# Kernel tuning notes

Measured on AMD Instinct MI355X. Metric: run time of the kernel, lower is better.

The kernel has to match this reference:

```python
import jax, jax.numpy as jnp
import numpy as np

DIM = 384
HEADS = 12
K = 3          # kernel_size
PAD = 1
STRIDE = 1
B, H, W = 8, 56, 56


def conv1x1(x, w, b=None):
    # x: [B,C,H,W], w: [O,C]
    y = jnp.einsum('bchw,oc->bohw', x, w)
    if b is not None:
        y = y + b[None, :, None, None]
    return y


def unfold(x, k, p, s):
    # torch nn.Unfold: returns patches [B, C, k*k, nH, nW], kernel row-major, channel-major overall
    Bx, C, Hx, Wx = x.shape
    nH = (Hx + 2 * p - k) // s + 1
    nW = (Wx + 2 * p - k) // s + 1
    xp = jnp.pad(x, ((0, 0), (0, 0), (p, p), (p, p)))
    cols = [xp[:, :, i:i + s * nH:s, j:j + s * nW:s] for i in range(k) for j in range(k)]
    return jnp.stack(cols, axis=2), nH, nW


def fold(col, Hx, Wx, k, p, s):
    # torch F.fold (col2im): scatter-add overlapping windows. col: [B, C, k*k, nH, nW]
    Bx, C, _, nH, nW = col.shape
    canvas = jnp.zeros((Bx, C, Hx + 2 * p, Wx + 2 * p), col.dtype)
    idx = 0
    for i in range(k):
        for j in range(k):
            canvas = canvas.at[:, :, i:i + s * nH:s, j:j + s * nW:s].add(col[:, :, idx])
            idx += 1
    return canvas[:, :, p:p + Hx, p:p + Wx]


def setup_inputs() -> dict:
    key = jax.random.key(0)
    ks = jax.random.split(key, 5)
    k2 = K * K
    x = jax.random.normal(ks[0], (B, DIM, H, W), dtype=jnp.float32)
    v_w = jax.random.normal(ks[1], (DIM, DIM), dtype=jnp.float32) * 0.02
    v_b = jnp.zeros((DIM,), dtype=jnp.float32)
    attn_w = jax.random.normal(ks[2], (k2 * k2 * HEADS, DIM), dtype=jnp.float32) * 0.02
    proj_w = jax.random.normal(ks[3], (DIM, DIM), dtype=jnp.float32) * 0.02
    return {'x': x, 'v_w': v_w, 'v_b': v_b, 'attn_w': attn_w, 'proj_w': proj_w}


def reference(x, v_w, v_b, attn_w, proj_w):
    Bx, C, Hx, Wx = x.shape
    k2 = K * K
    hd = C // HEADS  # head dim
    # value projection + unfold into overlapping k x k windows
    v = conv1x1(x, v_w, v_b)
    vcol, nH, nW = unfold(v, K, PAD, STRIDE)        # [B, C, k2, nH, nW]
    L = nH * nW
    v = vcol.reshape(Bx, HEADS, hd, k2, L)          # split C = (heads, hd), heads slow
    v = v.transpose(0, 1, 4, 3, 2)                  # [B, n, L, k2(d), hd]
    # adaptive avg pool to (nH, nW); with stride=1 this is identity (pool window 1)
    ph, pw = Hx // nH, Wx // nW
    xp = x.reshape(Bx, C, nH, ph, nW, pw).mean(axis=(3, 5))
    # per-pixel attention logits, channel layout = ((i*k2 + d)*HEADS + head)
    a = jnp.einsum('bchw,oc->bohw', xp, attn_w)     # [B, k2*k2*n, nH, nW]
    a = a.reshape(Bx, k2, k2, HEADS, L)             # [B, i, d, n, L]
    a = a.transpose(0, 3, 4, 1, 2)                  # [B, n, L, i, d]
    a = jax.nn.softmax(a, axis=-1)
    out = jnp.einsum('bnlid,bnldh->bnlih', a, v)    # [B, n, L, i, hd]
    out = out.transpose(0, 1, 4, 3, 2)              # [B, n, hd, i, L] -> channel (n*hd+h)
    out = out.reshape(Bx, C, k2, nH, nW)
    out = fold(out, Hx, Wx, K, PAD, STRIDE)         # scatter-add windows back
    return conv1x1(out, proj_w)
```

## Files before the change

### kernel.cpp

```cpp
#include <hip/hip_runtime.h>
#include <hip/hip_bf16.h>

#define DIM   384
#define HEADS 12
#define K2    9
#define HH    56
#define WW    56
#define HWP   3136
#define BB    8
#define AO    972
#define AOP   976
#define MCAT  1408
#define PP    3200
#define PPAD  3600
#define W60   60

#define WBLK     2688
#define HALOBLK  696

typedef __hip_bfloat16 bf16;
typedef short bf16x8 __attribute__((ext_vector_type(8)));
typedef short bf16x4v __attribute__((ext_vector_type(4)));
typedef float f32x4 __attribute__((ext_vector_type(4)));
typedef float f32x2 __attribute__((ext_vector_type(2)));

static __device__ __forceinline__ float b2f(bf16 v) { return __bfloat162float(v); }
static __device__ __forceinline__ float bs2f(short s) {
    return __uint_as_float(((unsigned int)(unsigned short)s) << 16);
}
static __device__ __forceinline__ short f2bs(float f) {
    __hip_bfloat16 h = __float2bfloat16(f);
    return *(short*)&h;
}
static __device__ __forceinline__ f32x2 unpk(unsigned int u) {
    f32x2 r;
    r[0] = __uint_as_float(u << 16);
    r[1] = __uint_as_float(u & 0xffff0000u);
    return r;
}

static __device__ __forceinline__ void gl_lds16(const bf16* g, bf16* l) {
    __builtin_amdgcn_global_load_lds(
        (const __attribute__((address_space(1))) unsigned int*)g,
        (__attribute__((address_space(3))) unsigned int*)l, 16, 0, 0);
}

__global__ __launch_bounds__(256) void prep_kernel(
        const float* __restrict__ x, const float* __restrict__ v_w,
        const float* __restrict__ attn_w, const float* __restrict__ proj_w,
        bf16* __restrict__ xT, bf16* __restrict__ wcat, bf16* __restrict__ wp,
        bf16* __restrict__ vP) {
    const int bid = blockIdx.x;
    if (bid < 400) {
        const int lane = threadIdx.x & 63, w = threadIdx.x >> 6;
        const int p = (bid % 50) * 64 + lane;
        const int b = bid / 50;
        bf16* dst = xT + ((size_t)b * PP + p) * DIM;
        if (p >= HWP) {
            bf16x8 z = {};
            for (int cg = w; cg < 48; cg += 4) *(bf16x8*)(dst + cg * 8) = z;
            return;
        }
        const float* src = x + (size_t)b * DIM * HWP + p;
        for (int cg = w; cg < 48; cg += 4) {
            bf16x8 v;
#pragma unroll
            for (int j = 0; j < 8; j++) v[j] = f2bs(src[(size_t)(cg * 8 + j) * HWP]);
            *(bf16x8*)(dst + cg * 8) = v;
        }
    } else if (bid < 400 + WBLK) {
        const int idx = (bid - 400) * 256 + threadIdx.x;
        const int NCAT = MCAT * DIM;
        if (idx < NCAT) {
            const int row = idx / DIM, col = idx % DIM;
            float v;
            if (row < 384) v = v_w[row * DIM + col];
            else {
                const int r2 = row - 384;
                if (r2 < AO) {
                    const int n = r2 / 81, rem = r2 % 81;
                    const int i = rem / 9, d = rem % 9;
                    v = attn_w[((i * 9 + d) * 12 + n) * DIM + col];
                } else v = 0.f;
            }
            *(short*)&wcat[idx] = f2bs(v);
        } else {
            const int j = idx - NCAT;
            if (j < 384 * DIM) *(short*)&wp[j] = f2bs(proj_w[j]);
        }
    } else {
        const int hidx = (bid - 400 - WBLK) * 256 + threadIdx.x;
        const int b = hidx / 22272;
        const int r = hidx % 22272;
        const int hp = r / 48, cgi = r % 48;
        int row, col;
        if (hp < 240) {
            const int rr = hp / 60;
            row = (rr < 2) ? rr : rr + 56;
            col = hp % 60;
        } else {
            const int h2 = hp - 240;
            row = 2 + (h2 >> 2);
            const int c4 = h2 & 3;
            col = (c4 < 2) ? c4 : c4 + 56;
        }
        bf16x8 z = {};
        *(bf16x8*)(vP + ((size_t)b * PPAD + row * W60 + col) * DIM + cgi * 8) = z;
    }
}

#define GEMM_STAGE(Ab, Bb, lA, lB, koff)                                       \
    {                                                                          \
        _Pragma("unroll")                                                      \
        for (int r = 0; r < 4; r++) {                                          \
            int idx = r * 256 + t;                                             \
            int row = idx >> 3;                                                \
            int kq = ((idx & 7) - (row >> 1)) & 7;                             \
            gl_lds16(Ab + (size_t)row * DIM + (koff) + kq * 8, lA + idx * 8);  \
        }                                                                      \
        _Pragma("unroll")                                                      \
        for (int r = 0; r < 4; r++) {                                          \
            int idx = r * 256 + t;                                             \
            int row = idx >> 3;                                                \
            int kq = ((idx & 7) - (row >> 1)) & 7;                             \
            gl_lds16(Bb + (size_t)row * DIM + (koff) + kq * 8, lB + idx * 8);  \
        }                                                                      \
    }

#define GEMM_COMPUTE(lA, lB, acc)                                              \
    __builtin_amdgcn_s_setprio(1);                                             \
    _Pragma("unroll")                                                          \
    for (int h = 0; h < 2; h++) {                                              \
        const int swzh = (((h << 2) + quad + (l16 >> 1)) & 7) * 8;             \
        bf16x8 af[4], bfr[4];                                                  \
        _Pragma("unroll")                                                      \
        for (int mt = 0; mt < 4; mt++)                                         \
            af[mt] = *(const bf16x8*)((lA) + (wm * 64 + mt * 16 + l16) * 64 + swzh); \
        _Pragma("unroll")                                                      \
        for (int nt = 0; nt < 4; nt++)                                         \
            bfr[nt] = *(const bf16x8*)((lB) + (wn * 64 + nt * 16 + l16) * 64 + swzh); \
        _Pragma("unroll")                                                      \
        for (int mt = 0; mt < 4; mt++)                                         \
            _Pragma("unroll")                                                  \
            for (int nt = 0; nt < 4; nt++)                                     \
                acc[mt][nt] = __builtin_amdgcn_mfma_f32_16x16x32_bf16(         \
                    af[mt], bfr[nt], acc[mt][nt], 0, 0, 0);                    \
    }                                                                          \
    __builtin_amdgcn_s_setprio(0);

#define GEMM_KSTEP(cA, cB, sA, sB, koff)                                       \
    GEMM_STAGE(Ab, Bb, sA, sB, koff)                                           \
    asm volatile("s_waitcnt vmcnt(8)" ::: "memory");                           \
    __builtin_amdgcn_s_barrier();                                              \
    GEMM_COMPUTE(cA, cB, acc)                                                  \
    asm volatile("s_waitcnt lgkmcnt(0)" ::: "memory");                         \
    __builtin_amdgcn_s_barrier();

#define GEMM_MAIN_LOOP_V6(Ab, Bb, acc)                                         \
    GEMM_STAGE(Ab, Bb, lA0, lB0, 0)                                            \
    GEMM_KSTEP(lA0, lB0, lA1, lB1, 64)                                         \
    GEMM_KSTEP(lA1, lB1, lA0, lB0, 128)                                        \
    GEMM_KSTEP(lA0, lB0, lA1, lB1, 192)                                        \
    GEMM_KSTEP(lA1, lB1, lA0, lB0, 256)                                        \
    GEMM_KSTEP(lA0, lB0, lA1, lB1, 320)                                        \
    asm volatile("s_waitcnt vmcnt(0)" ::: "memory");                           \
    __builtin_amdgcn_s_barrier();                                              \
    GEMM_COMPUTE(lA1, lB1, acc)

__global__ __launch_bounds__(256) void gemm12_kernel(
        const bf16* __restrict__ A, const bf16* __restrict__ Bt,
        const float* __restrict__ bias, bf16* __restrict__ vP,
        bf16* __restrict__ lT) {
    __shared__ bf16 lds[32768];
    bf16* lA0 = lds;
    bf16* lB0 = lds + 8192;
    bf16* lA1 = lds + 16384;
    bf16* lB1 = lds + 24576;
    const int t = threadIdx.x;
    const int lane = t & 63, w = t >> 6;
    const int wm = w & 1, wn = w >> 1;
    const int quad = lane >> 4, l16 = lane & 15;

    const int bid = blockIdx.x;
    const int swz = (bid & 7) * 275 + (bid >> 3);
    const int mtile = swz % 11;
    const int nb = swz / 11;
    const int ntile = nb % 25;
    const int b = nb / 25;
    const int n0 = ntile * 128;
    const int m0 = mtile * 128;

    const bf16* Ab = A + (size_t)m0 * DIM;
    const bf16* Bb = Bt + ((size_t)b * PP + n0) * DIM;

    f32x4 acc[4][4] = {};
    GEMM_MAIN_LOOP_V6(Ab, Bb, acc)

    const bool isv = (m0 < 384);
    const int ch0 = isv ? m0 : m0 - 384;

    bf16* wbuf = lds + w * 1152;
    const int nr = lane >> 2;
    const int mc = (lane & 3) * 16;
#pragma unroll
    for (int nt = 0; nt < 4; nt++) {
#pragma unroll
        for (int mt = 0; mt < 4; mt++) {
            float4 bi = make_float4(0.f, 0.f, 0.f, 0.f);
            if (isv) bi = *(const float4*)(bias + ch0 + wm * 64 + mt * 16 + quad * 4);
            bf16x4v pk;
            pk[0] = f2bs(acc[mt][nt][0] + bi.x);
            pk[1] = f2bs(acc[mt][nt][1] + bi.y);
            pk[2] = f2bs(acc[mt][nt][2] + bi.z);
            pk[3] = f2bs(acc[mt][nt][3] + bi.w);
            *(bf16x4v*)(wbuf + l16 * 72 + mt * 16 + quad * 4) = pk;
        }
        bf16x8 v0 = *(const bf16x8*)(wbuf + nr * 72 + mc);
        bf16x8 v1 = *(const bf16x8*)(wbuf + nr * 72 + mc + 8);
        const int p = n0 + wn * 64 + nt * 16 + nr;
        const int cc = ch0 + wm * 64 + mc;
        if (p < HWP && (isv || cc < AOP)) {
            bf16* dp;
            if (isv) {
                const int y = p / WW;
                dp = vP + ((size_t)b * PPAD + p + y * 4 + 122) * DIM + cc;
            } else {
                dp = lT + ((size_t)b * PP + p) * AOP + cc;
            }
            *(bf16x8*)dp = v0;
            *(bf16x8*)(dp + 8) = v1;
        }
    }
}

__global__ __launch_bounds__(256) void gemm_planar_kernel(
        const bf16* __restrict__ A, const bf16* __restrict__ Bt,
        float* __restrict__ out) {
    __shared__ bf16 lds[32768];
    bf16* lA0 = lds;
    bf16* lB0 = lds + 8192;
    bf16* lA1 = lds + 16384;
    bf16* lB1 = lds + 24576;
    const int t = threadIdx.x;
    const int lane = t & 63, w = t >> 6;
    const int wm = w & 1, wn = w >> 1;
    const int quad = lane >> 4, l16 = lane & 15;

    const int bid = blockIdx.x;
    const int swz = (bid & 7) * 75 + (bid >> 3);
    const int mtile = swz % 3;
    const int nb = swz / 3;
    const int ntile = nb % 25;
    const int b = nb / 25;
    const int n0 = ntile * 128;
    const int m0 = mtile * 128;

    const bf16* Ab = A + (size_t)m0 * DIM;
    const bf16* Bb = Bt + ((size_t)b * PP + n0) * DIM;

    f32x4 acc[4][4] = {};
    GEMM_MAIN_LOOP_V6(Ab, Bb, acc)

#pragma unroll
    for (int mt = 0; mt < 4; mt++) {
#pragma unroll
        for (int nt = 0; nt < 4; nt++) {
            int p = n0 + wn * 64 + nt * 16 + l16;
            if (p >= HWP) continue;
#pragma unroll
            for (int reg = 0; reg < 4; reg++) {
                int o = m0 + wm * 64 + mt * 16 + quad * 4 + reg;
                out[((size_t)b * DIM + o) * HWP + p] = acc[mt][nt][reg];
            }
        }
    }
}

__global__ __launch_bounds__(384) void attn_fold_kernel(
        const bf16* __restrict__ lT, const bf16* __restrict__ vP,
        bf16* __restrict__ cT) {
    __shared__ bf16 P[8 * 9 * 12 * 9];
    __shared__ float Wf[8 * 25 * 12];
    const int t = threadIdx.x;
    const int b = blockIdx.x & 7;
    const int pix0 = (blockIdx.x >> 3) * 8;
    const int Y = pix0 / WW, X0 = pix0 % WW;

    for (int r = t; r < 864; r += 384) {
        const int px = r / 108, rem = r % 108;
        const int i = rem / 12, n = rem % 12;
        const int ir = i / 3, ic = i % 3;
        const int yi = Y + 1 - ir, xi = X0 + px + 1 - ic;
        bf16* Pd = &P[r * 9];
        if (yi < 0 || yi >= HH || xi < 0 || xi >= WW) {
#pragma unroll
            for (int d = 0; d < K2; d++) *(short*)&Pd[d] = 0;
        } else {
            const bf16* base = lT + ((size_t)b * PP + yi * WW + xi) * AOP + n * 81 + i * 9;
            float lv[K2];
            float m = -1e30f;
#pragma unroll
            for (int d = 0; d < K2; d++) {
                lv[d] = b2f(base[d]);
                m = fmaxf(m, lv[d]);
            }
            float s = 0.f;
#pragma unroll
            for (int d = 0; d < K2; d++) { lv[d] = __expf(lv[d] - m); s += lv[d]; }
            const float inv = 1.f / s;
#pragma unroll
            for (int d = 0; d < K2; d++) *(short*)&Pd[d] = f2bs(lv[d] * inv);
        }
    }
    __syncthreads();

    if (t < 300) {
        const int off = t / 12, n = t % 12;
        const int dy = off / 5 - 2, dx = off % 5 - 2;
        const int ir_lo = max(0, -dy), ir_hi = min(2, 2 - dy);
        const int ic_lo = max(0, -dx), ic_hi = min(2, 2 - dx);
#pragma unroll
        for (int px = 0; px < 8; px++) {
            float wsum = 0.f;
            for (int ir = ir_lo; ir <= ir_hi; ir++)
                for (int ic = ic_lo; ic <= ic_hi; ic++) {
                    const int i = ir * 3 + ic;
                    const int d = (dy + ir) * 3 + (dx + ic);
                    wsum += b2f(P[((px * 9 + i) * 12 + n) * 9 + d]);
                }
            Wf[(px * 25 + off) * 12 + n] = wsum;
        }
    }
    __syncthreads();

    const int px = t / 48, cg = t % 48;
    const int X = X0 + px;
    const int n = cg >> 2;
    const float* Wp = &Wf[px * 300 + n];
    const bf16* vbp = vP + ((size_t)b * PPAD + (size_t)(Y + 2) * W60 + (X + 2)) * DIM + cg * 8;
    f32x2 a2[4] = {};
#pragma unroll
    for (int dy = -2; dy <= 2; dy++) {
        const bf16* rowb = vbp + dy * (W60 * DIM);
        const float* wrow = Wp + (dy + 2) * 60;
#pragma unroll
        for (int dx = -2; dx <= 2; dx++) {
            const float w = wrow[(dx + 2) * 12];
            const uint4 d = *(const uint4*)(rowb + dx * DIM);
            f32x2 w2; w2[0] = w; w2[1] = w;
            a2[0] = __builtin_elementwise_fma(unpk(d.x), w2, a2[0]);
            a2[1] = __builtin_elementwise_fma(unpk(d.y), w2, a2[1]);
            a2[2] = __builtin_elementwise_fma(unpk(d.z), w2, a2[2]);
            a2[3] = __builtin_elementwise_fma(unpk(d.w), w2, a2[3]);
        }
    }
    bf16x8 po;
#pragma unroll
    for (int j = 0; j < 4; j++) {
        po[2 * j]     = f2bs(a2[j][0]);
        po[2 * j + 1] = f2bs(a2[j][1]);
    }
    *(bf16x8*)(cT + ((size_t)b * PP + pix0 + px) * DIM + cg * 8) = po;
}

extern "C" void kernel_launch(void* const* d_in, const int* in_sizes, int n_in,
                              void* d_out, int out_size, void* d_ws, size_t ws_size,
                              hipStream_t stream) {
    const float* x      = (const float*)d_in[0];
    const float* v_w    = (const float*)d_in[1];
    const float* v_b    = (const float*)d_in[2];
    const float* attn_w = (const float*)d_in[3];
    const float* proj_w = (const float*)d_in[4];
    float* out = (float*)d_out;

    bf16* xT    = (bf16*)d_ws;
    bf16* vP    = xT + (size_t)BB * PP * DIM;
    bf16* lT    = vP + (size_t)BB * PPAD * DIM;
    bf16* wcat  = lT + (size_t)BB * PP * AOP;
    bf16* wp    = wcat + (size_t)MCAT * DIM;
    bf16* cT    = xT;

    const int nprep = 400 + WBLK + HALOBLK;
    prep_kernel<<<nprep, 256, 0, stream>>>(x, v_w, attn_w, proj_w, xT, wcat, wp, vP);

    gemm12_kernel<<<2200, 256, 0, stream>>>(wcat, xT, v_b, vP, lT);
    attn_fold_kernel<<<3136, 384, 0, stream>>>(lT, vP, cT);
    gemm_planar_kernel<<<600, 256, 0, stream>>>(wp, cT, out);
}
```

Measured before the change: 203.3 us.

## Enlarge gemm12 N-tile to 320 and drop double-buffered LDS pipeline

The fused value/logit GEMM now uses 128x320 output tiles (4x10 MFMA fragments per wave) instead of 128x128, cutting the grid from 2200 to 880 blocks so each A tile is reused across more columns. The double-buffered staged main loop is replaced by a simple single-buffer load/sync/compute loop. This reduces redundant A loads and block count but raises register pressure (160 accumulator floats) and loses load/compute overlap, and 880 blocks may underfill the GPU's compute units per wave.

```diff
diff --git a/kernel.cpp b/kernel.cpp
--- a/kernel.cpp
+++ b/kernel.cpp
@@ -167,34 +167,76 @@
     __builtin_amdgcn_s_barrier();                                              \
     GEMM_COMPUTE(lA1, lB1, acc)
 
+#define GEMM_STAGE10(Ab, Bb, lA, lB, koff)                                     \
+    {                                                                          \
+        _Pragma("unroll")                                                      \
+        for (int r = 0; r < 4; r++) {                                          \
+            int idx = r * 256 + t;                                             \
+            int row = idx >> 3;                                                \
+            int kq = ((idx & 7) - (row >> 1)) & 7;                             \
+            gl_lds16(Ab + (size_t)row * DIM + (koff) + kq * 8, lA + idx * 8);  \
+        }                                                                      \
+        _Pragma("unroll")                                                      \
+        for (int r = 0; r < 10; r++) {                                         \
+            int idx = r * 256 + t;                                             \
+            int row = idx >> 3;                                                \
+            int kq = ((idx & 7) - (row >> 1)) & 7;                             \
+            gl_lds16(Bb + (size_t)row * DIM + (koff) + kq * 8, lB + idx * 8);  \
+        }                                                                      \
+    }
+
+#define GEMM_COMPUTE10(lA, lB, acc)                                            \
+    __builtin_amdgcn_s_setprio(1);                                             \
+    _Pragma("unroll")                                                          \
+    for (int h = 0; h < 2; h++) {                                              \
+        const int swzh = (((h << 2) + quad + (l16 >> 1)) & 7) * 8;             \
+        bf16x8 af[4], bfr[10];                                                 \
+        _Pragma("unroll")                                                      \
+        for (int mt = 0; mt < 4; mt++)                                         \
+            af[mt] = *(const bf16x8*)((lA) + (wm * 64 + mt * 16 + l16) * 64 + swzh); \
+        _Pragma("unroll")                                                      \
+        for (int nt = 0; nt < 10; nt++)                                        \
+            bfr[nt] = *(const bf16x8*)((lB) + (wn * 160 + nt * 16 + l16) * 64 + swzh); \
+        _Pragma("unroll")                                                      \
+        for (int mt = 0; mt < 4; mt++)                                         \
+            _Pragma("unroll")                                                  \
+            for (int nt = 0; nt < 10; nt++)                                    \
+                acc[mt][nt] = __builtin_amdgcn_mfma_f32_16x16x32_bf16(         \
+                    af[mt], bfr[nt], acc[mt][nt], 0, 0, 0);                    \
+    }                                                                          \
+    __builtin_amdgcn_s_setprio(0);
+
 __global__ __launch_bounds__(256) void gemm12_kernel(
         const bf16* __restrict__ A, const bf16* __restrict__ Bt,
         const float* __restrict__ bias, bf16* __restrict__ vP,
         bf16* __restrict__ lT) {
-    __shared__ bf16 lds[32768];
-    bf16* lA0 = lds;
-    bf16* lB0 = lds + 8192;
-    bf16* lA1 = lds + 16384;
-    bf16* lB1 = lds + 24576;
+    __shared__ bf16 lds[28672];
+    bf16* lA = lds;
+    bf16* lB = lds + 8192;
     const int t = threadIdx.x;
     const int lane = t & 63, w = t >> 6;
     const int wm = w & 1, wn = w >> 1;
     const int quad = lane >> 4, l16 = lane & 15;
 
     const int bid = blockIdx.x;
-    const int swz = (bid & 7) * 275 + (bid >> 3);
+    const int swz = (bid & 7) * 110 + (bid >> 3);
     const int mtile = swz % 11;
     const int nb = swz / 11;
-    const int ntile = nb % 25;
-    const int b = nb / 25;
-    const int n0 = ntile * 128;
+    const int ntile = nb % 10;
+    const int b = nb / 10;
+    const int n0 = ntile * 320;
     const int m0 = mtile * 128;
 
     const bf16* Ab = A + (size_t)m0 * DIM;
     const bf16* Bb = Bt + ((size_t)b * PP + n0) * DIM;
 
-    f32x4 acc[4][4] = {};
-    GEMM_MAIN_LOOP_V6(Ab, Bb, acc)
+    f32x4 acc[4][10] = {};
+    for (int k0 = 0; k0 < DIM; k0 += 64) {
+        GEMM_STAGE10(Ab, Bb, lA, lB, k0)
+        __syncthreads();
+        GEMM_COMPUTE10(lA, lB, acc)
+        __syncthreads();
+    }
 
     const bool isv = (m0 < 384);
     const int ch0 = isv ? m0 : m0 - 384;
@@ -203,7 +245,7 @@
     const int nr = lane >> 2;
     const int mc = (lane & 3) * 16;
 #pragma unroll
-    for (int nt = 0; nt < 4; nt++) {
+    for (int nt = 0; nt < 10; nt++) {
 #pragma unroll
         for (int mt = 0; mt < 4; mt++) {
             float4 bi = make_float4(0.f, 0.f, 0.f, 0.f);
@@ -217,7 +259,7 @@
         }
         bf16x8 v0 = *(const bf16x8*)(wbuf + nr * 72 + mc);
         bf16x8 v1 = *(const bf16x8*)(wbuf + nr * 72 + mc + 8);
-        const int p = n0 + wn * 64 + nt * 16 + nr;
+        const int p = n0 + wn * 160 + nt * 16 + nr;
         const int cc = ch0 + wm * 64 + mc;
         if (p < HWP && (isv || cc < AOP)) {
             bf16* dp;
@@ -383,7 +425,7 @@
     const int nprep = 400 + WBLK + HALOBLK;
     prep_kernel<<<nprep, 256, 0, stream>>>(x, v_w, attn_w, proj_w, xT, wcat, wp, vP);
 
-    gemm12_kernel<<<2200, 256, 0, stream>>>(wcat, xT, v_b, vP, lT);
+    gemm12_kernel<<<880, 256, 0, stream>>>(wcat, xT, v_b, vP, lT);
     attn_fold_kernel<<<3136, 384, 0, stream>>>(lT, vP, cT);
     gemm_planar_kernel<<<600, 256, 0, stream>>>(wp, cT, out);
 }
```

Result: slower. 234.9 us (+15.6%).
